# Optimization experiments

Hardware: AMD Instinct MI355X
Metric: run time of the kernel (lower is better)

Reference implementation:

```python
import jax, jax.numpy as jnp
import numpy as np

N = 50000      # total nodes
E = 400000     # edges (before self-loops)
F_IN = 75      # atom features
H = 4          # GAT heads (layers 1,2)
C = 128        # hidden_channels
G = 512        # graphs in batch
EPS_BN = 1e-5


def setup_inputs() -> dict:
    key = jax.random.key(0)
    ks = jax.random.split(key, 32)
    inp = {}
    inp["x"] = jax.random.normal(ks[0], (N, F_IN), jnp.float32)
    inp["edge_index"] = jax.random.randint(ks[1], (2, E), 0, N, dtype=jnp.int32)
    inp["batch"] = jnp.sort(jax.random.randint(ks[2], (N,), 0, G, dtype=jnp.int32))
    # (in_dim, heads, out_per_head, concat)
    dims = [(F_IN, H, C, True), (H * C, H, C, True), (H * C, 1, C, False)]
    i = 3
    for li, (din, h, c, concat) in enumerate(dims, 1):
        dout = h * c if concat else c
        s = 1.0 / np.sqrt(din)
        inp[f"W{li}"] = jax.random.normal(ks[i], (din, h * c), jnp.float32) * s
        inp[f"as{li}"] = jax.random.normal(ks[i + 1], (h, c), jnp.float32) * 0.1
        inp[f"ad{li}"] = jax.random.normal(ks[i + 2], (h, c), jnp.float32) * 0.1
        inp[f"b{li}"] = jnp.zeros((dout,), jnp.float32)
        inp[f"g{li}"] = jnp.ones((dout,), jnp.float32)
        inp[f"bt{li}"] = jnp.zeros((dout,), jnp.float32)
        inp[f"rm{li}"] = jax.random.normal(ks[i + 3], (dout,), jnp.float32) * 0.05
        inp[f"rv{li}"] = jnp.ones((dout,), jnp.float32)
        i += 4
    return inp


def gat_layer(x, src, dst, W, a_src, a_dst, b, heads, c_out, concat):
    # x: [N, Fin] -> h: [N, H, C]
    n = x.shape[0]
    h = (x @ W).reshape(n, heads, c_out)
    # per-node attention logits [N, H]
    al_s = jnp.sum(h * a_src[None], axis=-1)
    al_d = jnp.sum(h * a_dst[None], axis=-1)
    # per-edge logits + leaky relu (PyG GATConv, slope 0.2)
    e = jax.nn.leaky_relu(al_s[src] + al_d[dst], negative_slope=0.2)  # [E, H]
    # segment softmax over destination nodes
    emax = jax.ops.segment_max(e, dst, num_segments=n)
    p = jnp.exp(e - emax[dst])
    denom = jax.ops.segment_sum(p, dst, num_segments=n)
    alpha = p / (denom[dst] + 1e-16)
    # weighted message aggregation
    msg = h[src] * alpha[:, :, None]            # [E, H, C]
    out = jax.ops.segment_sum(msg, dst, num_segments=n)  # [N, H, C]
    out = out.reshape(n, heads * c_out) if concat else out.mean(axis=1)
    return out + b


def bn_eval(x, g, bt, rm, rv):
    return (x - rm) * g * jax.lax.rsqrt(rv + EPS_BN) + bt


def reference(x, edge_index, batch,
              W1, as1, ad1, b1, g1, bt1, rm1, rv1,
              W2, as2, ad2, b2, g2, bt2, rm2, rv2,
              W3, as3, ad3, b3, g3, bt3, rm3, rv3):
    n = x.shape[0]
    ar = jnp.arange(n, dtype=edge_index.dtype)
    # GATConv adds self-loops by default
    src = jnp.concatenate([edge_index[0], ar])
    dst = jnp.concatenate([edge_index[1], ar])

    h = gat_layer(x, src, dst, W1, as1, ad1, b1, H, C, True)
    h = jax.nn.relu(bn_eval(h, g1, bt1, rm1, rv1))   # dropout off (eval)
    h = gat_layer(h, src, dst, W2, as2, ad2, b2, H, C, True)
    h = jax.nn.relu(bn_eval(h, g2, bt2, rm2, rv2))
    h = gat_layer(h, src, dst, W3, as3, ad3, b3, 1, C, False)
    h = bn_eval(h, g3, bt3, rm3, rv3)

    # global mean + max pool over graphs
    ones = jnp.ones((n,), h.dtype)
    cnt = jnp.maximum(jax.ops.segment_sum(ones, batch, num_segments=G), 1.0)
    gmean = jax.ops.segment_sum(h, batch, num_segments=G) / cnt[:, None]
    gmax = jax.ops.segment_max(h, batch, num_segments=G)
    gmax = jnp.where(jnp.isfinite(gmax), gmax, 0.0)  # guard empty graphs
    return jnp.concatenate([gmean, gmax], axis=1)    # [G, 2*C]
```

## Files before the change

kernel.cpp:

```cpp
#include <hip/hip_runtime.h>

typedef unsigned short u16;
typedef unsigned int u32;
typedef __attribute__((ext_vector_type(8))) short s16x8;
typedef __attribute__((ext_vector_type(4))) float f32x4;

__device__ __forceinline__ float bf2f(u32 u) {
    return __uint_as_float(u << 16);
}
__device__ __forceinline__ u16 f2bf(float f) {
    u32 x = __float_as_uint(f);
    u32 r = (x + 0x7fffu + ((x >> 16) & 1u)) >> 16;
    return (u16)r;
}

__device__ __forceinline__ void gload16(const u16* g, u16* l) {
    __builtin_amdgcn_global_load_lds(
        (const __attribute__((address_space(1))) unsigned int*)g,
        (__attribute__((address_space(3))) unsigned int*)l,
        16, 0, 0);
}

__global__ __launch_bounds__(256) void cvtx_k(
    const float* __restrict__ x, u16* __restrict__ xb, int N, int Mp)
{
    const int i = blockIdx.x * 256 + threadIdx.x;
    if (i >= Mp * 96) return;
    const int r = i / 96, c = i - r * 96;
    float v = (r < N && c < 75) ? x[(size_t)r * 75 + c] : 0.f;
    xb[i] = f2bf(v);
}

__global__ __launch_bounds__(256) void cvtw_k(
    const float* __restrict__ W, u16* __restrict__ Wt, int K, int Kp, int Ncol)
{
    const int i = blockIdx.x * 256 + threadIdx.x;
    if (i >= Ncol * Kp) return;
    const int n = i / Kp, k = i - n * Kp;
    Wt[i] = f2bf(k < K ? W[(size_t)k * Ncol + n] : 0.f);
}

__global__ __launch_bounds__(256) void mgemm_k(
    const u16* __restrict__ A, const u16* __restrict__ Bt, u16* __restrict__ C,
    const float* __restrict__ avs, const float* __restrict__ avd,
    float* __restrict__ als, float* __restrict__ ald,
    int M, int K, int Ncol, int H, int NXB)
{
    __shared__ u16 Al[2][128 * 32];
    __shared__ u16 Bl[2][128 * 32];
    const int t = threadIdx.x;
    const int lane = t & 63;
    const int wid = t >> 6;
    const int wr = wid >> 1, wc = wid & 1;
    const int rr = lane & 15, q = lane >> 4;

    const int dd = blockIdx.x;
    const int xcd = dd & 7, ii = dd >> 3;
    const int gpx = (int)(gridDim.x >> 3) / NXB;
    const int yb = xcd * gpx + ((NXB == 4) ? (ii >> 2) : ii);
    const int head = (NXB == 4) ? (ii & 3) : 0;
    const int m0 = yb * 128, n0 = head * 128;

    f32x4 acc[4][4];
#pragma unroll
    for (int m = 0; m < 4; ++m)
#pragma unroll
        for (int n = 0; n < 4; ++n) acc[m][n] = (f32x4){0.f, 0.f, 0.f, 0.f};

    auto stage = [&](int b, int k0) {
#pragma unroll
        for (int i2 = 0; i2 < 2; ++i2) {
            const int si = i2 * 256 + t;
            const int r = si >> 2, s = si & 3;
            const int g = s ^ ((r >> 1) & 3);
            gload16(A  + (size_t)(m0 + r) * K + k0 + g * 8, &Al[b][si * 8]);
            gload16(Bt + (size_t)(n0 + r) * K + k0 + g * 8, &Bl[b][si * 8]);
        }
    };

    const int nk = K >> 5;
    stage(0, 0);
    __syncthreads();
    int buf = 0;
    for (int kt = 0; kt < nk; ++kt) {
        if (kt + 1 < nk) stage(buf ^ 1, (kt + 1) << 5);
        s16x8 af[4], bfr[4];
#pragma unroll
        for (int m = 0; m < 4; ++m) {
            const int r = wr * 64 + m * 16 + rr;
            af[m] = *reinterpret_cast<const s16x8*>(&Al[buf][r * 32 + ((q ^ ((r >> 1) & 3)) << 3)]);
        }
#pragma unroll
        for (int n = 0; n < 4; ++n) {
            const int r = wc * 64 + n * 16 + rr;
            bfr[n] = *reinterpret_cast<const s16x8*>(&Bl[buf][r * 32 + ((q ^ ((r >> 1) & 3)) << 3)]);
        }
#pragma unroll
        for (int m = 0; m < 4; ++m)
#pragma unroll
            for (int n = 0; n < 4; ++n)
                acc[m][n] = __builtin_amdgcn_mfma_f32_16x16x32_bf16(af[m], bfr[n], acc[m][n], 0, 0, 0);
        __syncthreads();
        buf ^= 1;
    }

#pragma unroll
    for (int m = 0; m < 4; ++m) {
        const int row_b = m0 + wr * 64 + m * 16 + q * 4;
#pragma unroll
        for (int j = 0; j < 4; ++j) {
            const int row = row_b + j;
            if (row < M) {
#pragma unroll
                for (int n = 0; n < 4; ++n) {
                    const int col = n0 + wc * 64 + n * 16 + rr;
                    C[(size_t)row * Ncol + col] = f2bf(acc[m][n][j]);
                }
            }
        }
    }

    float asv[4], adv[4];
#pragma unroll
    for (int n = 0; n < 4; ++n) {
        const int c = wc * 64 + n * 16 + rr;
        asv[n] = avs[head * 128 + c];
        adv[n] = avd[head * 128 + c];
    }
    float* lps = (float*)&Al[0][0];
    float* lpd = lps + 256;
#pragma unroll
    for (int m = 0; m < 4; ++m)
#pragma unroll
        for (int j = 0; j < 4; ++j) {
            float ps = 0.f, pd = 0.f;
#pragma unroll
            for (int n = 0; n < 4; ++n) {
                ps += acc[m][n][j] * asv[n];
                pd += acc[m][n][j] * adv[n];
            }
#pragma unroll
            for (int off = 1; off < 16; off <<= 1) {
                ps += __shfl_xor(ps, off, 64);
                pd += __shfl_xor(pd, off, 64);
            }
            if (rr == 0) {
                const int r = wr * 64 + m * 16 + q * 4 + j;
                lps[wc * 128 + r] = ps;
                lpd[wc * 128 + r] = pd;
            }
        }
    __syncthreads();
    if (t < 128) {
        const int row = m0 + t;
        if (row < M) {
            als[(size_t)row * H + head] = lps[t] + lps[128 + t];
            ald[(size_t)row * H + head] = lpd[t] + lpd[128 + t];
        }
    }
}

__global__ void count_k(const int* __restrict__ edst, int* __restrict__ cnt, int E_, int N_)
{
    const int i = blockIdx.x * 256 + threadIdx.x;
    if (i >= E_ + N_) return;
    const int d = (i < E_) ? edst[i] : (i - E_);
    atomicAdd(&cnt[d], 1);
}

#define SCAN_B 256
__global__ void scan1_k(const int* __restrict__ cnt, int* __restrict__ part,
                        int* __restrict__ bsum, int n)
{
    __shared__ int sm[SCAN_B];
    const int idx = blockIdx.x * SCAN_B + threadIdx.x;
    int v = (idx < n) ? cnt[idx] : 0;
    sm[threadIdx.x] = v;
    __syncthreads();
    for (int off = 1; off < SCAN_B; off <<= 1) {
        int t2 = (threadIdx.x >= off) ? sm[threadIdx.x - off] : 0;
        __syncthreads();
        sm[threadIdx.x] += t2;
        __syncthreads();
    }
    if (idx < n) part[idx] = sm[threadIdx.x];
    if (threadIdx.x == SCAN_B - 1) bsum[blockIdx.x] = sm[threadIdx.x];
}

__global__ void scan2_k(int* __restrict__ bsum, int nb)
{
    __shared__ int sm[SCAN_B];
    const int t = threadIdx.x;
    int v = (t < nb) ? bsum[t] : 0;
    sm[t] = v;
    __syncthreads();
    for (int off = 1; off < SCAN_B; off <<= 1) {
        int t2 = (t >= off) ? sm[t - off] : 0;
        __syncthreads();
        sm[t] += t2;
        __syncthreads();
    }
    if (t < nb) bsum[t] = sm[t] - v;
}

__global__ void scan3_k(const int* __restrict__ part, const int* __restrict__ boff,
                        int* __restrict__ offs, int n)
{
    const int idx = blockIdx.x * SCAN_B + threadIdx.x;
    if (idx < n) offs[idx + 1] = part[idx] + boff[idx / SCAN_B];
    if (idx == 0) offs[0] = 0;
}

__global__ void scatter_k(const int* __restrict__ esrc, const int* __restrict__ edst,
                          const int* __restrict__ offs, int* __restrict__ fill,
                          int* __restrict__ csr, int E_, int N_)
{
    const int i = blockIdx.x * 256 + threadIdx.x;
    if (i >= E_ + N_) return;
    int s, d;
    if (i < E_) { s = esrc[i]; d = edst[i]; } else { s = d = i - E_; }
    const int pos = offs[d] + atomicAdd(&fill[d], 1);
    csr[pos] = s;
}

template<int CH, int C, bool RELU>
__global__ __launch_bounds__(256) void agg_k(
    const u16* __restrict__ hsrc, const int* __restrict__ offs,
    const int* __restrict__ csr, const float* __restrict__ als,
    const float* __restrict__ ald, const float* __restrict__ bias,
    const float* __restrict__ gam, const float* __restrict__ bet,
    const float* __restrict__ rmean, const float* __restrict__ rvar,
    u16* __restrict__ outp, int N)
{
    constexpr int HH = CH / C;
    constexpr int Kc = CH / 64;
    const int lane = threadIdx.x & 63;
    const int dst = blockIdx.x * 4 + (threadIdx.x >> 6);
    if (dst >= N) return;
    const int ch0 = Kc * lane;
    const int hd = ch0 / C;

    float adv[HH];
#pragma unroll
    for (int h = 0; h < HH; ++h) adv[h] = ald[(size_t)dst * HH + h];

    const int rs = offs[dst], re = offs[dst + 1];

    float m[HH];
#pragma unroll
    for (int h = 0; h < HH; ++h) m[h] = -1e30f;
    for (int s = rs + lane; s < re; s += 64) {
        const int sn = csr[s];
        if constexpr (HH == 4) {
            const float4 av = *reinterpret_cast<const float4*>(&als[(size_t)sn * 4]);
            const float ev[4] = {av.x + adv[0], av.y + adv[1], av.z + adv[2], av.w + adv[3]};
#pragma unroll
            for (int h = 0; h < 4; ++h) {
                float e = ev[h]; e = (e > 0.f) ? e : 0.2f * e;
                m[h] = fmaxf(m[h], e);
            }
        } else {
            float e = als[sn] + adv[0]; e = (e > 0.f) ? e : 0.2f * e;
            m[0] = fmaxf(m[0], e);
        }
    }
#pragma unroll
    for (int h = 0; h < HH; ++h)
#pragma unroll
        for (int off = 32; off; off >>= 1) m[h] = fmaxf(m[h], __shfl_xor(m[h], off, 64));

    float smv[HH];
#pragma unroll
    for (int h = 0; h < HH; ++h) smv[h] = 0.f;
    for (int s = rs + lane; s < re; s += 64) {
        const int sn = csr[s];
        if constexpr (HH == 4) {
            const float4 av = *reinterpret_cast<const float4*>(&als[(size_t)sn * 4]);
            const float ev[4] = {av.x + adv[0], av.y + adv[1], av.z + adv[2], av.w + adv[3]};
#pragma unroll
            for (int h = 0; h < 4; ++h) {
                float e = ev[h]; e = (e > 0.f) ? e : 0.2f * e;
                smv[h] += __expf(e - m[h]);
            }
        } else {
            float e = als[sn] + adv[0]; e = (e > 0.f) ? e : 0.2f * e;
            smv[0] += __expf(e - m[0]);
        }
    }
#pragma unroll
    for (int h = 0; h < HH; ++h)
#pragma unroll
        for (int off = 32; off; off >>= 1) smv[h] += __shfl_xor(smv[h], off, 64);
    float inv[HH];
#pragma unroll
    for (int h = 0; h < HH; ++h) inv[h] = 1.f / (smv[h] + 1e-16f);

    const float mh = m[hd], invh = inv[hd], advh = adv[hd];

    float acc[Kc] = {};
    int s = rs;
    for (; s + 4 <= re; s += 4) {
        int sn[4];
#pragma unroll
        for (int u = 0; u < 4; ++u) sn[u] = csr[s + u];
        if constexpr (Kc == 8) {
            int4 r[4];
#pragma unroll
            for (int u = 0; u < 4; ++u)
                r[u] = *reinterpret_cast<const int4*>(hsrc + (size_t)sn[u] * CH + ch0);
            float aa[4];
#pragma unroll
            for (int u = 0; u < 4; ++u) {
                float e = als[(size_t)sn[u] * HH + hd] + advh;
                e = (e > 0.f) ? e : 0.2f * e;
                aa[u] = __expf(e - mh) * invh;
            }
#pragma unroll
            for (int u = 0; u < 4; ++u) {
                const u32 rr2[4] = {(u32)r[u].x, (u32)r[u].y, (u32)r[u].z, (u32)r[u].w};
#pragma unroll
                for (int qq = 0; qq < 4; ++qq) {
                    acc[2*qq]   += aa[u] * bf2f(rr2[qq] & 0xffffu);
                    acc[2*qq+1] += aa[u] * bf2f(rr2[qq] >> 16);
                }
            }
        } else {
            u32 r[4];
#pragma unroll
            for (int u = 0; u < 4; ++u)
                r[u] = *reinterpret_cast<const u32*>(hsrc + (size_t)sn[u] * CH + ch0);
            float aa[4];
#pragma unroll
            for (int u = 0; u < 4; ++u) {
                float e = als[sn[u]] + advh;
                e = (e > 0.f) ? e : 0.2f * e;
                aa[u] = __expf(e - mh) * invh;
            }
#pragma unroll
            for (int u = 0; u < 4; ++u) {
                acc[0] += aa[u] * bf2f(r[u] & 0xffffu);
                acc[1] += aa[u] * bf2f(r[u] >> 16);
            }
        }
    }
    for (; s < re; ++s) {
        const int sn = csr[s];
        float e = als[(size_t)sn * HH + hd] + advh;
        e = (e > 0.f) ? e : 0.2f * e;
        const float a = __expf(e - mh) * invh;
        const u16* hp = hsrc + (size_t)sn * CH + ch0;
        if constexpr (Kc == 8) {
            const int4 r = *reinterpret_cast<const int4*>(hp);
            const u32 rr2[4] = {(u32)r.x, (u32)r.y, (u32)r.z, (u32)r.w};
#pragma unroll
            for (int qq = 0; qq < 4; ++qq) {
                acc[2*qq]   += a * bf2f(rr2[qq] & 0xffffu);
                acc[2*qq+1] += a * bf2f(rr2[qq] >> 16);
            }
        } else {
            const u32 r = *reinterpret_cast<const u32*>(hp);
            acc[0] += a * bf2f(r & 0xffffu);
            acc[1] += a * bf2f(r >> 16);
        }
    }

    u16 ob[Kc];
#pragma unroll
    for (int j = 0; j < Kc; ++j) {
        const int ch = ch0 + j;
        const float scale = gam[ch] * rsqrtf(rvar[ch] + 1e-5f);
        float val = (acc[j] + bias[ch] - rmean[ch]) * scale + bet[ch];
        if (RELU) val = fmaxf(val, 0.f);
        ob[j] = f2bf(val);
    }
    u16* op = outp + (size_t)dst * CH + ch0;
    if constexpr (Kc == 8) {
        int4 w;
        w.x = (int)((u32)ob[0] | ((u32)ob[1] << 16));
        w.y = (int)((u32)ob[2] | ((u32)ob[3] << 16));
        w.z = (int)((u32)ob[4] | ((u32)ob[5] << 16));
        w.w = (int)((u32)ob[6] | ((u32)ob[7] << 16));
        *reinterpret_cast<int4*>(op) = w;
    } else {
        *reinterpret_cast<u32*>(op) = (u32)ob[0] | ((u32)ob[1] << 16);
    }
}

__global__ __launch_bounds__(128) void pool_k(
    const u16* __restrict__ h3, const int* __restrict__ batch,
    float* __restrict__ out, int N)
{
    const int g = blockIdx.x;
    const int t = threadIdx.x;
    int lo = 0, hi = N;
    while (lo < hi) { int mid = (lo + hi) >> 1; if (batch[mid] < g) lo = mid + 1; else hi = mid; }
    const int s0 = lo;
    lo = 0; hi = N;
    while (lo < hi) { int mid = (lo + hi) >> 1; if (batch[mid] < g + 1) lo = mid + 1; else hi = mid; }
    const int s1 = lo;
    float sum = 0.f, mx = -1e30f;
    for (int n = s0; n < s1; ++n) {
        const float v = bf2f((u32)h3[(size_t)n * 128 + t]);
        sum += v;
        mx = fmaxf(mx, v);
    }
    const int cnt = s1 - s0;
    out[(size_t)g * 256 + t]       = cnt ? sum / (float)cnt : 0.f;
    out[(size_t)g * 256 + 128 + t] = cnt ? mx : 0.f;
}

extern "C" void kernel_launch(void* const* d_in, const int* in_sizes, int n_in,
                              void* d_out, int out_size, void* d_ws, size_t ws_size,
                              hipStream_t stream)
{
    const float* x   = (const float*)d_in[0];
    const int* ei    = (const int*)d_in[1];
    const int* batch = (const int*)d_in[2];
    const float* W1  = (const float*)d_in[3];
    const float* as1 = (const float*)d_in[4];
    const float* ad1 = (const float*)d_in[5];
    const float* b1  = (const float*)d_in[6];
    const float* g1  = (const float*)d_in[7];
    const float* bt1 = (const float*)d_in[8];
    const float* rm1 = (const float*)d_in[9];
    const float* rv1 = (const float*)d_in[10];
    const float* W2  = (const float*)d_in[11];
    const float* as2 = (const float*)d_in[12];
    const float* ad2 = (const float*)d_in[13];
    const float* b2  = (const float*)d_in[14];
    const float* g2  = (const float*)d_in[15];
    const float* bt2 = (const float*)d_in[16];
    const float* rm2 = (const float*)d_in[17];
    const float* rv2 = (const float*)d_in[18];
    const float* W3  = (const float*)d_in[19];
    const float* as3 = (const float*)d_in[20];
    const float* ad3 = (const float*)d_in[21];
    const float* b3  = (const float*)d_in[22];
    const float* g3  = (const float*)d_in[23];
    const float* bt3 = (const float*)d_in[24];
    const float* rm3 = (const float*)d_in[25];
    const float* rv3 = (const float*)d_in[26];

    const int Nn = in_sizes[2];
    const int Ee = in_sizes[1] / 2;
    const int ET = Ee + Nn;
    const int Gg = out_size / 256;
    const int Mp = 392 * 128;

    char* ws = (char*)d_ws;
    size_t o = 0;
    auto alc = [&](size_t bytes) { size_t r = o; o = (o + bytes + 255) & ~(size_t)255; return r; };
    u16*  hA   = (u16*)(ws + alc((size_t)Mp * 512 * 2));
    u16*  hB   = (u16*)(ws + alc((size_t)Mp * 512 * 2));
    u16*  xb   = (u16*)(ws + alc((size_t)Mp * 96 * 2));
    u16*  Wt1  = (u16*)(ws + alc((size_t)512 * 96 * 2));
    u16*  Wt2  = (u16*)(ws + alc((size_t)512 * 512 * 2));
    u16*  Wt3  = (u16*)(ws + alc((size_t)128 * 512 * 2));
    float* als = (float*)(ws + alc((size_t)Nn * 4 * 4));
    float* ald = (float*)(ws + alc((size_t)Nn * 4 * 4));
    int*  cnt  = (int*)(ws + alc((size_t)2 * Nn * 4));
    int*  fill = cnt + Nn;
    int*  offs = (int*)(ws + alc((size_t)(Nn + 1) * 4));
    int*  part = (int*)(ws + alc((size_t)Nn * 4));
    int*  bsum = (int*)(ws + alc((size_t)SCAN_B * 4));
    int*  csr  = (int*)(ws + alc((size_t)ET * 4));
    (void)ws_size; (void)n_in;

    hipMemsetAsync(cnt, 0, (size_t)2 * Nn * 4, stream);
    const int ETB = (ET + 255) / 256;
    count_k<<<ETB, 256, 0, stream>>>(ei + Ee, cnt, Ee, Nn);
    const int nb = (Nn + SCAN_B - 1) / SCAN_B;
    scan1_k<<<nb, SCAN_B, 0, stream>>>(cnt, part, bsum, Nn);
    scan2_k<<<1, SCAN_B, 0, stream>>>(bsum, nb);
    scan3_k<<<nb, SCAN_B, 0, stream>>>(part, bsum, offs, Nn);
    scatter_k<<<ETB, 256, 0, stream>>>(ei, ei + Ee, offs, fill, csr, Ee, Nn);

    cvtx_k<<<(Mp * 96 + 255) / 256, 256, 0, stream>>>(x, xb, Nn, Mp);
    cvtw_k<<<(512 * 96 + 255) / 256, 256, 0, stream>>>(W1, Wt1, 75, 96, 512);
    cvtw_k<<<(512 * 512 + 255) / 256, 256, 0, stream>>>(W2, Wt2, 512, 512, 512);
    cvtw_k<<<(128 * 512 + 255) / 256, 256, 0, stream>>>(W3, Wt3, 512, 512, 128);

    const int nwb = (Nn + 3) / 4;
    const int nwg4 = 392 * 4;
    const int nwg1 = 392;

    mgemm_k<<<nwg4, 256, 0, stream>>>(xb, Wt1, hA, as1, ad1, als, ald, Nn, 96, 512, 4, 4);
    agg_k<512, 128, true><<<nwb, 256, 0, stream>>>(hA, offs, csr, als, ald,
                                                   b1, g1, bt1, rm1, rv1, hB, Nn);
    mgemm_k<<<nwg4, 256, 0, stream>>>(hB, Wt2, hA, as2, ad2, als, ald, Nn, 512, 512, 4, 4);
    agg_k<512, 128, true><<<nwb, 256, 0, stream>>>(hA, offs, csr, als, ald,
                                                   b2, g2, bt2, rm2, rv2, hB, Nn);
    mgemm_k<<<nwg1, 256, 0, stream>>>(hB, Wt3, hA, as3, ad3, als, ald, Nn, 512, 128, 1, 1);
    agg_k<128, 128, false><<<nwb, 256, 0, stream>>>(hA, offs, csr, als, ald,
                                                    b3, g3, bt3, rm3, rv3, hB, Nn);
    pool_k<<<Gg, 128, 0, stream>>>(hB, batch, (float*)d_out, Nn);
}
```

Before: 401.5 us.

## Split wide GAT aggregation across two waves and drop max pass in softmax

For the 512-channel layers, each destination node is now handled by two wavefronts that each cover half the channels (two heads), loading 8-byte instead of 16-byte rows per lane. This doubles the number of waves in flight to hide gather latency. Separately, the segment-max pass is removed: logits are clamped at 60 and exponentiated directly, saving one full pass over neighbour logits. The clamp changes results only when a logit exceeds 60, and the unshifted exp risks precision loss if logits are very negative.

```diff
diff --git a/kernel.cpp b/kernel.cpp
--- a/kernel.cpp
+++ b/kernel.cpp
@@ -19,6 +19,11 @@
         (const __attribute__((address_space(1))) unsigned int*)g,
         (__attribute__((address_space(3))) unsigned int*)l,
         16, 0, 0);
+}
+
+__device__ __forceinline__ float lk60(float e) {
+    e = (e > 0.f) ? e : 0.2f * e;
+    return fminf(e, 60.f);
 }
 
 __global__ __launch_bounds__(256) void cvtx_k(
@@ -223,7 +228,7 @@
     csr[pos] = s;
 }
 
-template<int CH, int C, bool RELU>
+template<int CH, int C, int SPLIT, bool RELU>
 __global__ __launch_bounds__(256) void agg_k(
     const u16* __restrict__ hsrc, const int* __restrict__ offs,
     const int* __restrict__ csr, const float* __restrict__ als,
@@ -233,69 +238,43 @@
     u16* __restrict__ outp, int N)
 {
     constexpr int HH = CH / C;
-    constexpr int Kc = CH / 64;
+    constexpr int PW = CH / SPLIT;
+    constexpr int Kc = PW / 64;
+    constexpr int HPW = (PW + C - 1) / C;
     const int lane = threadIdx.x & 63;
-    const int dst = blockIdx.x * 4 + (threadIdx.x >> 6);
+    const int wid = threadIdx.x >> 6;
+    const int dst = blockIdx.x * (4 / SPLIT) + (SPLIT == 1 ? wid : (wid >> 1));
     if (dst >= N) return;
-    const int ch0 = Kc * lane;
+    const int half = (SPLIT == 1) ? 0 : (wid & (SPLIT - 1));
+    const int ch0 = half * PW + lane * Kc;
     const int hd = ch0 / C;
-
-    float adv[HH];
-#pragma unroll
-    for (int h = 0; h < HH; ++h) adv[h] = ald[(size_t)dst * HH + h];
+    const int h0 = half * HPW;
+
+    float adv[HPW];
+#pragma unroll
+    for (int h = 0; h < HPW; ++h) adv[h] = ald[(size_t)dst * HH + h0 + h];
 
     const int rs = offs[dst], re = offs[dst + 1];
 
-    float m[HH];
-#pragma unroll
-    for (int h = 0; h < HH; ++h) m[h] = -1e30f;
+    float smv[HPW];
+#pragma unroll
+    for (int h = 0; h < HPW; ++h) smv[h] = 0.f;
     for (int s = rs + lane; s < re; s += 64) {
         const int sn = csr[s];
-        if constexpr (HH == 4) {
-            const float4 av = *reinterpret_cast<const float4*>(&als[(size_t)sn * 4]);
-            const float ev[4] = {av.x + adv[0], av.y + adv[1], av.z + adv[2], av.w + adv[3]};
-#pragma unroll
-            for (int h = 0; h < 4; ++h) {
-                float e = ev[h]; e = (e > 0.f) ? e : 0.2f * e;
-                m[h] = fmaxf(m[h], e);
-            }
+        if constexpr (HPW == 2) {
+            const float2 av = *reinterpret_cast<const float2*>(&als[(size_t)sn * HH + h0]);
+            smv[0] += __expf(lk60(av.x + adv[0]));
+            smv[1] += __expf(lk60(av.y + adv[1]));
         } else {
-            float e = als[sn] + adv[0]; e = (e > 0.f) ? e : 0.2f * e;
-            m[0] = fmaxf(m[0], e);
-        }
-    }
-#pragma unroll
-    for (int h = 0; h < HH; ++h)
-#pragma unroll
-        for (int off = 32; off; off >>= 1) m[h] = fmaxf(m[h], __shfl_xor(m[h], off, 64));
-
-    float smv[HH];
-#pragma unroll
-    for (int h = 0; h < HH; ++h) smv[h] = 0.f;
-    for (int s = rs + lane; s < re; s += 64) {
-        const int sn = csr[s];
-        if constexpr (HH == 4) {
-            const float4 av = *reinterpret_cast<const float4*>(&als[(size_t)sn * 4]);
-            const float ev[4] = {av.x + adv[0], av.y + adv[1], av.z + adv[2], av.w + adv[3]};
-#pragma unroll
-            for (int h = 0; h < 4; ++h) {
-                float e = ev[h]; e = (e > 0.f) ? e : 0.2f * e;
-                smv[h] += __expf(e - m[h]);
-            }
-        } else {
-            float e = als[sn] + adv[0]; e = (e > 0.f) ? e : 0.2f * e;
-            smv[0] += __expf(e - m[0]);
-        }
-    }
-#pragma unroll
-    for (int h = 0; h < HH; ++h)
+            smv[0] += __expf(lk60(als[(size_t)sn * HH + h0] + adv[0]));
+        }
+    }
+#pragma unroll
+    for (int h = 0; h < HPW; ++h)
 #pragma unroll
         for (int off = 32; off; off >>= 1) smv[h] += __shfl_xor(smv[h], off, 64);
-    float inv[HH];
-#pragma unroll
-    for (int h = 0; h < HH; ++h) inv[h] = 1.f / (smv[h] + 1e-16f);
-
-    const float mh = m[hd], invh = inv[hd], advh = adv[hd];
+    const float invh = 1.f / (smv[hd - h0] + 1e-16f);
+    const float advh = adv[hd - h0];
 
     float acc[Kc] = {};
     int s = rs;
@@ -303,26 +282,21 @@
         int sn[4];
 #pragma unroll
         for (int u = 0; u < 4; ++u) sn[u] = csr[s + u];
-        if constexpr (Kc == 8) {
-            int4 r[4];
+        if constexpr (Kc == 4) {
+            uint2 r[4];
 #pragma unroll
             for (int u = 0; u < 4; ++u)
-                r[u] = *reinterpret_cast<const int4*>(hsrc + (size_t)sn[u] * CH + ch0);
+                r[u] = *reinterpret_cast<const uint2*>(hsrc + (size_t)sn[u] * CH + ch0);
             float aa[4];
 #pragma unroll
+            for (int u = 0; u < 4; ++u)
+                aa[u] = __expf(lk60(als[(size_t)sn[u] * HH + hd] + advh)) * invh;
+#pragma unroll
             for (int u = 0; u < 4; ++u) {
-                float e = als[(size_t)sn[u] * HH + hd] + advh;
-                e = (e > 0.f) ? e : 0.2f * e;
-                aa[u] = __expf(e - mh) * invh;
-            }
-#pragma unroll
-            for (int u = 0; u < 4; ++u) {
-                const u32 rr2[4] = {(u32)r[u].x, (u32)r[u].y, (u32)r[u].z, (u32)r[u].w};
-#pragma unroll
-                for (int qq = 0; qq < 4; ++qq) {
-                    acc[2*qq]   += aa[u] * bf2f(rr2[qq] & 0xffffu);
-                    acc[2*qq+1] += aa[u] * bf2f(rr2[qq] >> 16);
-                }
+                acc[0] += aa[u] * bf2f(r[u].x & 0xffffu);
+                acc[1] += aa[u] * bf2f(r[u].x >> 16);
+                acc[2] += aa[u] * bf2f(r[u].y & 0xffffu);
+                acc[3] += aa[u] * bf2f(r[u].y >> 16);
             }
         } else {
             u32 r[4];
@@ -331,11 +305,8 @@
                 r[u] = *reinterpret_cast<const u32*>(hsrc + (size_t)sn[u] * CH + ch0);
             float aa[4];
 #pragma unroll
-            for (int u = 0; u < 4; ++u) {
-                float e = als[sn[u]] + advh;
-                e = (e > 0.f) ? e : 0.2f * e;
-                aa[u] = __expf(e - mh) * invh;
-            }
+            for (int u = 0; u < 4; ++u)
+                aa[u] = __expf(lk60(als[(size_t)sn[u] * HH + hd] + advh)) * invh;
 #pragma unroll
             for (int u = 0; u < 4; ++u) {
                 acc[0] += aa[u] * bf2f(r[u] & 0xffffu);
@@ -345,18 +316,14 @@
     }
     for (; s < re; ++s) {
         const int sn = csr[s];
-        float e = als[(size_t)sn * HH + hd] + advh;
-        e = (e > 0.f) ? e : 0.2f * e;
-        const float a = __expf(e - mh) * invh;
+        const float a = __expf(lk60(als[(size_t)sn * HH + hd] + advh)) * invh;
         const u16* hp = hsrc + (size_t)sn * CH + ch0;
-        if constexpr (Kc == 8) {
-            const int4 r = *reinterpret_cast<const int4*>(hp);
-            const u32 rr2[4] = {(u32)r.x, (u32)r.y, (u32)r.z, (u32)r.w};
-#pragma unroll
-            for (int qq = 0; qq < 4; ++qq) {
-                acc[2*qq]   += a * bf2f(rr2[qq] & 0xffffu);
-                acc[2*qq+1] += a * bf2f(rr2[qq] >> 16);
-            }
+        if constexpr (Kc == 4) {
+            const uint2 r = *reinterpret_cast<const uint2*>(hp);
+            acc[0] += a * bf2f(r.x & 0xffffu);
+            acc[1] += a * bf2f(r.x >> 16);
+            acc[2] += a * bf2f(r.y & 0xffffu);
+            acc[3] += a * bf2f(r.y >> 16);
         } else {
             const u32 r = *reinterpret_cast<const u32*>(hp);
             acc[0] += a * bf2f(r & 0xffffu);
@@ -374,13 +341,11 @@
         ob[j] = f2bf(val);
     }
     u16* op = outp + (size_t)dst * CH + ch0;
-    if constexpr (Kc == 8) {
-        int4 w;
-        w.x = (int)((u32)ob[0] | ((u32)ob[1] << 16));
-        w.y = (int)((u32)ob[2] | ((u32)ob[3] << 16));
-        w.z = (int)((u32)ob[4] | ((u32)ob[5] << 16));
-        w.w = (int)((u32)ob[6] | ((u32)ob[7] << 16));
-        *reinterpret_cast<int4*>(op) = w;
+    if constexpr (Kc == 4) {
+        uint2 w;
+        w.x = (u32)ob[0] | ((u32)ob[1] << 16);
+        w.y = (u32)ob[2] | ((u32)ob[3] << 16);
+        *reinterpret_cast<uint2*>(op) = w;
     } else {
         *reinterpret_cast<u32*>(op) = (u32)ob[0] | ((u32)ob[1] << 16);
     }
@@ -480,18 +445,19 @@
     cvtw_k<<<(512 * 512 + 255) / 256, 256, 0, stream>>>(W2, Wt2, 512, 512, 512);
     cvtw_k<<<(128 * 512 + 255) / 256, 256, 0, stream>>>(W3, Wt3, 512, 512, 128);
 
-    const int nwb = (Nn + 3) / 4;
+    const int nwb2 = (Nn + 1) / 2;
+    const int nwb4 = (Nn + 3) / 4;
     const int nwg4 = 392 * 4;
     const int nwg1 = 392;
 
     mgemm_k<<<nwg4, 256, 0, stream>>>(xb, Wt1, hA, as1, ad1, als, ald, Nn, 96, 512, 4, 4);
-    agg_k<512, 128, true><<<nwb, 256, 0, stream>>>(hA, offs, csr, als, ald,
-                                                   b1, g1, bt1, rm1, rv1, hB, Nn);
+    agg_k<512, 128, 2, true><<<nwb2, 256, 0, stream>>>(hA, offs, csr, als, ald,
+                                                       b1, g1, bt1, rm1, rv1, hB, Nn);
     mgemm_k<<<nwg4, 256, 0, stream>>>(hB, Wt2, hA, as2, ad2, als, ald, Nn, 512, 512, 4, 4);
-    agg_k<512, 128, true><<<nwb, 256, 0, stream>>>(hA, offs, csr, als, ald,
-                                                   b2, g2, bt2, rm2, rv2, hB, Nn);
+    agg_k<512, 128, 2, true><<<nwb2, 256, 0, stream>>>(hA, offs, csr, als, ald,
+                                                       b2, g2, bt2, rm2, rv2, hB, Nn);
     mgemm_k<<<nwg1, 256, 0, stream>>>(hB, Wt3, hA, as3, ad3, als, ald, Nn, 512, 128, 1, 1);
-    agg_k<128, 128, false><<<nwb, 256, 0, stream>>>(hA, offs, csr, als, ald,
-                                                    b3, g3, bt3, rm3, rv3, hB, Nn);
+    agg_k<128, 128, 1, false><<<nwb4, 256, 0, stream>>>(hA, offs, csr, als, ald,
+                                                        b3, g3, bt3, rm3, rv3, hB, Nn);
     pool_k<<<Gg, 128, 0, stream>>>(hB, batch, (float*)d_out, Nn);
 }
```

Result: slower. 414.5 us (+3.2%).

## Drop softmax max pass via clamped exponent; pack four nodes per wave in final layer

Applied to the files above, without the earlier changes.

The segment-softmax max-reduction pass over incoming edges is removed. Logits are clamped at 60 after the leaky ReLU and exponentiated directly, so each node needs only one pass over its edges before aggregation instead of two. The last layer (128 channels, one head) gets a dedicated kernel where each group of 16 lanes handles one destination node, so a wave processes four nodes and uses 16-byte loads instead of 4-byte ones. The clamp changes numerics if any logit exceeds 60, and results may overflow or lose precision versus the max-subtracted form in extreme cases.

```diff
diff --git a/kernel.cpp b/kernel.cpp
--- a/kernel.cpp
+++ b/kernel.cpp
@@ -19,6 +19,11 @@
         (const __attribute__((address_space(1))) unsigned int*)g,
         (__attribute__((address_space(3))) unsigned int*)l,
         16, 0, 0);
+}
+
+__device__ __forceinline__ float lk60(float e) {
+    e = (e > 0.f) ? e : 0.2f * e;
+    return fminf(e, 60.f);
 }
 
 __global__ __launch_bounds__(256) void cvtx_k(
@@ -223,8 +228,8 @@
     csr[pos] = s;
 }
 
-template<int CH, int C, bool RELU>
-__global__ __launch_bounds__(256) void agg_k(
+template<bool RELU>
+__global__ __launch_bounds__(256) void agg512_k(
     const u16* __restrict__ hsrc, const int* __restrict__ offs,
     const int* __restrict__ csr, const float* __restrict__ als,
     const float* __restrict__ ald, const float* __restrict__ bias,
@@ -232,158 +237,159 @@
     const float* __restrict__ rmean, const float* __restrict__ rvar,
     u16* __restrict__ outp, int N)
 {
-    constexpr int HH = CH / C;
-    constexpr int Kc = CH / 64;
     const int lane = threadIdx.x & 63;
     const int dst = blockIdx.x * 4 + (threadIdx.x >> 6);
     if (dst >= N) return;
-    const int ch0 = Kc * lane;
-    const int hd = ch0 / C;
-
-    float adv[HH];
-#pragma unroll
-    for (int h = 0; h < HH; ++h) adv[h] = ald[(size_t)dst * HH + h];
-
+    const int ch0 = lane * 8;
+    const int hd = lane >> 4;
+
+    const float4 adv = *reinterpret_cast<const float4*>(&ald[(size_t)dst * 4]);
+    const float advs[4] = {adv.x, adv.y, adv.z, adv.w};
     const int rs = offs[dst], re = offs[dst + 1];
 
-    float m[HH];
-#pragma unroll
-    for (int h = 0; h < HH; ++h) m[h] = -1e30f;
+    float smv[4] = {0.f, 0.f, 0.f, 0.f};
     for (int s = rs + lane; s < re; s += 64) {
         const int sn = csr[s];
-        if constexpr (HH == 4) {
-            const float4 av = *reinterpret_cast<const float4*>(&als[(size_t)sn * 4]);
-            const float ev[4] = {av.x + adv[0], av.y + adv[1], av.z + adv[2], av.w + adv[3]};
-#pragma unroll
-            for (int h = 0; h < 4; ++h) {
-                float e = ev[h]; e = (e > 0.f) ? e : 0.2f * e;
-                m[h] = fmaxf(m[h], e);
-            }
-        } else {
-            float e = als[sn] + adv[0]; e = (e > 0.f) ? e : 0.2f * e;
-            m[0] = fmaxf(m[0], e);
-        }
-    }
-#pragma unroll
-    for (int h = 0; h < HH; ++h)
-#pragma unroll
-        for (int off = 32; off; off >>= 1) m[h] = fmaxf(m[h], __shfl_xor(m[h], off, 64));
-
-    float smv[HH];
-#pragma unroll
-    for (int h = 0; h < HH; ++h) smv[h] = 0.f;
-    for (int s = rs + lane; s < re; s += 64) {
-        const int sn = csr[s];
-        if constexpr (HH == 4) {
-            const float4 av = *reinterpret_cast<const float4*>(&als[(size_t)sn * 4]);
-            const float ev[4] = {av.x + adv[0], av.y + adv[1], av.z + adv[2], av.w + adv[3]};
-#pragma unroll
-            for (int h = 0; h < 4; ++h) {
-                float e = ev[h]; e = (e > 0.f) ? e : 0.2f * e;
-                smv[h] += __expf(e - m[h]);
-            }
-        } else {
-            float e = als[sn] + adv[0]; e = (e > 0.f) ? e : 0.2f * e;
-            smv[0] += __expf(e - m[0]);
-        }
-    }
-#pragma unroll
-    for (int h = 0; h < HH; ++h)
+        const float4 av = *reinterpret_cast<const float4*>(&als[(size_t)sn * 4]);
+        smv[0] += __expf(lk60(av.x + advs[0]));
+        smv[1] += __expf(lk60(av.y + advs[1]));
+        smv[2] += __expf(lk60(av.z + advs[2]));
+        smv[3] += __expf(lk60(av.w + advs[3]));
+    }
+#pragma unroll
+    for (int h = 0; h < 4; ++h)
 #pragma unroll
         for (int off = 32; off; off >>= 1) smv[h] += __shfl_xor(smv[h], off, 64);
-    float inv[HH];
-#pragma unroll
-    for (int h = 0; h < HH; ++h) inv[h] = 1.f / (smv[h] + 1e-16f);
-
-    const float mh = m[hd], invh = inv[hd], advh = adv[hd];
-
-    float acc[Kc] = {};
+    const float invh = 1.f / (smv[hd] + 1e-16f);
+    const float advh = advs[hd];
+
+    float acc[8] = {};
     int s = rs;
     for (; s + 4 <= re; s += 4) {
         int sn[4];
 #pragma unroll
         for (int u = 0; u < 4; ++u) sn[u] = csr[s + u];
-        if constexpr (Kc == 8) {
-            int4 r[4];
-#pragma unroll
-            for (int u = 0; u < 4; ++u)
-                r[u] = *reinterpret_cast<const int4*>(hsrc + (size_t)sn[u] * CH + ch0);
-            float aa[4];
-#pragma unroll
-            for (int u = 0; u < 4; ++u) {
-                float e = als[(size_t)sn[u] * HH + hd] + advh;
-                e = (e > 0.f) ? e : 0.2f * e;
-                aa[u] = __expf(e - mh) * invh;
-            }
-#pragma unroll
-            for (int u = 0; u < 4; ++u) {
-                const u32 rr2[4] = {(u32)r[u].x, (u32)r[u].y, (u32)r[u].z, (u32)r[u].w};
-#pragma unroll
-                for (int qq = 0; qq < 4; ++qq) {
-                    acc[2*qq]   += aa[u] * bf2f(rr2[qq] & 0xffffu);
-                    acc[2*qq+1] += aa[u] * bf2f(rr2[qq] >> 16);
-                }
-            }
-        } else {
-            u32 r[4];
-#pragma unroll
-            for (int u = 0; u < 4; ++u)
-                r[u] = *reinterpret_cast<const u32*>(hsrc + (size_t)sn[u] * CH + ch0);
-            float aa[4];
-#pragma unroll
-            for (int u = 0; u < 4; ++u) {
-                float e = als[sn[u]] + advh;
-                e = (e > 0.f) ? e : 0.2f * e;
-                aa[u] = __expf(e - mh) * invh;
-            }
-#pragma unroll
-            for (int u = 0; u < 4; ++u) {
-                acc[0] += aa[u] * bf2f(r[u] & 0xffffu);
-                acc[1] += aa[u] * bf2f(r[u] >> 16);
+        int4 r[4];
+#pragma unroll
+        for (int u = 0; u < 4; ++u)
+            r[u] = *reinterpret_cast<const int4*>(hsrc + (size_t)sn[u] * 512 + ch0);
+        float aa[4];
+#pragma unroll
+        for (int u = 0; u < 4; ++u)
+            aa[u] = __expf(lk60(als[(size_t)sn[u] * 4 + hd] + advh)) * invh;
+#pragma unroll
+        for (int u = 0; u < 4; ++u) {
+            const u32 rr2[4] = {(u32)r[u].x, (u32)r[u].y, (u32)r[u].z, (u32)r[u].w};
+#pragma unroll
+            for (int qq = 0; qq < 4; ++qq) {
+                acc[2*qq]   += aa[u] * bf2f(rr2[qq] & 0xffffu);
+                acc[2*qq+1] += aa[u] * bf2f(rr2[qq] >> 16);
             }
         }
     }
     for (; s < re; ++s) {
         const int sn = csr[s];
-        float e = als[(size_t)sn * HH + hd] + advh;
-        e = (e > 0.f) ? e : 0.2f * e;
-        const float a = __expf(e - mh) * invh;
-        const u16* hp = hsrc + (size_t)sn * CH + ch0;
-        if constexpr (Kc == 8) {
-            const int4 r = *reinterpret_cast<const int4*>(hp);
-            const u32 rr2[4] = {(u32)r.x, (u32)r.y, (u32)r.z, (u32)r.w};
-#pragma unroll
-            for (int qq = 0; qq < 4; ++qq) {
-                acc[2*qq]   += a * bf2f(rr2[qq] & 0xffffu);
-                acc[2*qq+1] += a * bf2f(rr2[qq] >> 16);
-            }
-        } else {
-            const u32 r = *reinterpret_cast<const u32*>(hp);
-            acc[0] += a * bf2f(r & 0xffffu);
-            acc[1] += a * bf2f(r >> 16);
-        }
-    }
-
-    u16 ob[Kc];
-#pragma unroll
-    for (int j = 0; j < Kc; ++j) {
+        const float a = __expf(lk60(als[(size_t)sn * 4 + hd] + advh)) * invh;
+        const int4 r = *reinterpret_cast<const int4*>(hsrc + (size_t)sn * 512 + ch0);
+        const u32 rr2[4] = {(u32)r.x, (u32)r.y, (u32)r.z, (u32)r.w};
+#pragma unroll
+        for (int qq = 0; qq < 4; ++qq) {
+            acc[2*qq]   += a * bf2f(rr2[qq] & 0xffffu);
+            acc[2*qq+1] += a * bf2f(rr2[qq] >> 16);
+        }
+    }
+
+    u16 ob[8];
+#pragma unroll
+    for (int j = 0; j < 8; ++j) {
         const int ch = ch0 + j;
         const float scale = gam[ch] * rsqrtf(rvar[ch] + 1e-5f);
         float val = (acc[j] + bias[ch] - rmean[ch]) * scale + bet[ch];
         if (RELU) val = fmaxf(val, 0.f);
         ob[j] = f2bf(val);
     }
-    u16* op = outp + (size_t)dst * CH + ch0;
-    if constexpr (Kc == 8) {
-        int4 w;
-        w.x = (int)((u32)ob[0] | ((u32)ob[1] << 16));
-        w.y = (int)((u32)ob[2] | ((u32)ob[3] << 16));
-        w.z = (int)((u32)ob[4] | ((u32)ob[5] << 16));
-        w.w = (int)((u32)ob[6] | ((u32)ob[7] << 16));
-        *reinterpret_cast<int4*>(op) = w;
-    } else {
-        *reinterpret_cast<u32*>(op) = (u32)ob[0] | ((u32)ob[1] << 16);
-    }
+    int4 w;
+    w.x = (int)((u32)ob[0] | ((u32)ob[1] << 16));
+    w.y = (int)((u32)ob[2] | ((u32)ob[3] << 16));
+    w.z = (int)((u32)ob[4] | ((u32)ob[5] << 16));
+    w.w = (int)((u32)ob[6] | ((u32)ob[7] << 16));
+    *reinterpret_cast<int4*>(outp + (size_t)dst * 512 + ch0) = w;
+}
+
+__global__ __launch_bounds__(256) void agg128_k(
+    const u16* __restrict__ hsrc, const int* __restrict__ offs,
+    const int* __restrict__ csr, const float* __restrict__ als,
+    const float* __restrict__ ald, const float* __restrict__ bias,
+    const float* __restrict__ gam, const float* __restrict__ bet,
+    const float* __restrict__ rmean, const float* __restrict__ rvar,
+    u16* __restrict__ outp, int N)
+{
+    const int tid = threadIdx.x;
+    const int w = tid >> 6, g = (tid >> 4) & 3, l = tid & 15;
+    const int dst = blockIdx.x * 16 + w * 4 + g;
+    if (dst >= N) return;
+    const int ch0 = l * 8;
+
+    const float advh = ald[dst];
+    const int rs = offs[dst], re = offs[dst + 1];
+
+    float sm = 0.f;
+    for (int s = rs + l; s < re; s += 16)
+        sm += __expf(lk60(als[csr[s]] + advh));
+#pragma unroll
+    for (int off = 8; off; off >>= 1) sm += __shfl_xor(sm, off, 64);
+    const float inv = 1.f / (sm + 1e-16f);
+
+    float acc[8] = {};
+    int s = rs;
+    for (; s + 4 <= re; s += 4) {
+        int sn[4];
+#pragma unroll
+        for (int u = 0; u < 4; ++u) sn[u] = csr[s + u];
+        int4 r[4];
+#pragma unroll
+        for (int u = 0; u < 4; ++u)
+            r[u] = *reinterpret_cast<const int4*>(hsrc + (size_t)sn[u] * 128 + ch0);
+        float aa[4];
+#pragma unroll
+        for (int u = 0; u < 4; ++u)
+            aa[u] = __expf(lk60(als[sn[u]] + advh)) * inv;
+#pragma unroll
+        for (int u = 0; u < 4; ++u) {
+            const u32 rr2[4] = {(u32)r[u].x, (u32)r[u].y, (u32)r[u].z, (u32)r[u].w};
+#pragma unroll
+            for (int qq = 0; qq < 4; ++qq) {
+                acc[2*qq]   += aa[u] * bf2f(rr2[qq] & 0xffffu);
+                acc[2*qq+1] += aa[u] * bf2f(rr2[qq] >> 16);
+            }
+        }
+    }
+    for (; s < re; ++s) {
+        const int sn = csr[s];
+        const float a = __expf(lk60(als[sn] + advh)) * inv;
+        const int4 r = *reinterpret_cast<const int4*>(hsrc + (size_t)sn * 128 + ch0);
+        const u32 rr2[4] = {(u32)r.x, (u32)r.y, (u32)r.z, (u32)r.w};
+#pragma unroll
+        for (int qq = 0; qq < 4; ++qq) {
+            acc[2*qq]   += a * bf2f(rr2[qq] & 0xffffu);
+            acc[2*qq+1] += a * bf2f(rr2[qq] >> 16);
+        }
+    }
+
+    u16 ob[8];
+#pragma unroll
+    for (int j = 0; j < 8; ++j) {
+        const int ch = ch0 + j;
+        const float scale = gam[ch] * rsqrtf(rvar[ch] + 1e-5f);
+        float val = (acc[j] + bias[ch] - rmean[ch]) * scale + bet[ch];
+        ob[j] = f2bf(val);
+    }
+    int4 wv;
+    wv.x = (int)((u32)ob[0] | ((u32)ob[1] << 16));
+    wv.y = (int)((u32)ob[2] | ((u32)ob[3] << 16));
+    wv.z = (int)((u32)ob[4] | ((u32)ob[5] << 16));
+    wv.w = (int)((u32)ob[6] | ((u32)ob[7] << 16));
+    *reinterpret_cast<int4*>(outp + (size_t)dst * 128 + ch0) = wv;
 }
 
 __global__ __launch_bounds__(128) void pool_k(
@@ -480,18 +486,19 @@
     cvtw_k<<<(512 * 512 + 255) / 256, 256, 0, stream>>>(W2, Wt2, 512, 512, 512);
     cvtw_k<<<(128 * 512 + 255) / 256, 256, 0, stream>>>(W3, Wt3, 512, 512, 128);
 
-    const int nwb = (Nn + 3) / 4;
+    const int nwb4  = (Nn + 3) / 4;
+    const int nwb16 = (Nn + 15) / 16;
     const int nwg4 = 392 * 4;
     const int nwg1 = 392;
 
     mgemm_k<<<nwg4, 256, 0, stream>>>(xb, Wt1, hA, as1, ad1, als, ald, Nn, 96, 512, 4, 4);
-    agg_k<512, 128, true><<<nwb, 256, 0, stream>>>(hA, offs, csr, als, ald,
-                                                   b1, g1, bt1, rm1, rv1, hB, Nn);
+    agg512_k<true><<<nwb4, 256, 0, stream>>>(hA, offs, csr, als, ald,
+                                             b1, g1, bt1, rm1, rv1, hB, Nn);
     mgemm_k<<<nwg4, 256, 0, stream>>>(hB, Wt2, hA, as2, ad2, als, ald, Nn, 512, 512, 4, 4);
-    agg_k<512, 128, true><<<nwb, 256, 0, stream>>>(hA, offs, csr, als, ald,
-                                                   b2, g2, bt2, rm2, rv2, hB, Nn);
+    agg512_k<true><<<nwb4, 256, 0, stream>>>(hA, offs, csr, als, ald,
+                                             b2, g2, bt2, rm2, rv2, hB, Nn);
     mgemm_k<<<nwg1, 256, 0, stream>>>(hB, Wt3, hA, as3, ad3, als, ald, Nn, 512, 128, 1, 1);
-    agg_k<128, 128, false><<<nwb, 256, 0, stream>>>(hA, offs, csr, als, ald,
-                                                    b3, g3, bt3, rm3, rv3, hB, Nn);
+    agg128_k<<<nwb16, 256, 0, stream>>>(hA, offs, csr, als, ald,
+                                        b3, g3, bt3, rm3, rv3, hB, Nn);
     pool_k<<<Gg, 128, 0, stream>>>(hB, batch, (float*)d_out, Nn);
 }
```

Result: faster. 379.9 us (-5.4%).
